# Optimization experiments

Measured on AMD Instinct MI355X. Metric: run time of the kernel, lower is better.

The kernel has to match this reference:

```python
import jax, jax.numpy as jnp
import numpy as np

B, C = 8192, 4096
P, Q, EPS = 0.8, 2.0, 0.01


def setup_inputs() -> dict:
    key = jax.random.key(0)
    k1, k2 = jax.random.split(key)
    outputs = jax.random.normal(k1, (B, C), dtype=jnp.float32)
    targets = jax.random.randint(k2, (B,), 0, C)
    return {"outputs": outputs, "targets": targets}


def reference(outputs, targets):
    num_classes = outputs.shape[1]
    # accumulated class counts for this batch (torch loop over unique targets == bincount)
    acc = jax.ops.segment_sum(
        jnp.ones_like(targets, dtype=outputs.dtype), targets, num_segments=num_classes
    )
    acc = jnp.clip(acc, 1.0)  # clamp(min=1)
    onehot = jax.nn.one_hot(targets, num_classes, dtype=outputs.dtype)  # [B, C]

    # mitigation factor: gather rows of the implicit CxC ratio matrix by target
    # ratio[b, j] = acc[j] / acc[targets[b]]
    ratio = acc[None, :] / acc[targets][:, None]  # [B, C]
    mitigation = jnp.where(ratio < 1.0, ratio ** P, 1.0)

    # compensation factor on detached softmax scores
    scores = jax.nn.softmax(jax.lax.stop_gradient(outputs), axis=1)  # [B, C]
    self_scores = jnp.take_along_axis(scores, targets[:, None], axis=1)  # [B, 1]
    sratio = scores / jnp.clip(self_scores, EPS)
    compensation = jnp.where(sratio > 1.0, sratio ** Q, 1.0)

    seesaw = mitigation * compensation  # [B, C]
    logits = outputs + jnp.log(seesaw) * (1.0 - onehot)

    logp = jax.nn.log_softmax(logits, axis=1)
    nll = -jnp.take_along_axis(logp, targets[:, None], axis=1)[:, 0]
    return jnp.mean(nll)
```

## Files before the change

kernel.cpp:

```cpp
#include <hip/hip_runtime.h>
#include <math.h>


#define CC 4096

__device__ __forceinline__ float wave_max(float v) {
    #pragma unroll
    for (int o = 32; o > 0; o >>= 1) v = fmaxf(v, __shfl_xor(v, o, 64));
    return v;
}
__device__ __forceinline__ float wave_sum(float v) {
    #pragma unroll
    for (int o = 32; o > 0; o >>= 1) v += __shfl_xor(v, o, 64);
    return v;
}

__device__ __forceinline__ float exp4(float4& v, float m) {
    v.x = __expf(v.x - m); v.y = __expf(v.y - m);
    v.z = __expf(v.z - m); v.w = __expf(v.w - m);
    return (v.x + v.y) + (v.z + v.w);
}

__device__ __forceinline__ float zsum4(float4 e, float4 pa, float rt, float c) {
    float gx = e.x * c, gy = e.y * c, gz = e.z * c, gw = e.w * c;
    float hx = fmaxf(gx * gx * gx, gx), hy = fmaxf(gy * gy * gy, gy);
    float hz = fmaxf(gz * gz * gz, gz), hw = fmaxf(gw * gw * gw, gw);
    float mx = fminf(pa.x * rt, 1.f),  my = fminf(pa.y * rt, 1.f);
    float mz = fminf(pa.z * rt, 1.f),  mw = fminf(pa.w * rt, 1.f);
    return (hx * mx + hy * my) + (hz * mz + hw * mw);
}

__global__ __launch_bounds__(1024) void k_hist(const int* __restrict__ tg, int B,
                                               float* __restrict__ powacc) {
    __shared__ int hacc[CC];
    const int tid = threadIdx.x;
    #pragma unroll
    for (int k = 0; k < CC / 1024; ++k) hacc[tid + k * 1024] = 0;
    __syncthreads();
    const int4* __restrict__ tg4 = (const int4*)tg;
    for (int i = tid; i < B / 4; i += 1024) {
        int4 tv = tg4[i];
        atomicAdd(&hacc[tv.x], 1); atomicAdd(&hacc[tv.y], 1);
        atomicAdd(&hacc[tv.z], 1); atomicAdd(&hacc[tv.w], 1);
    }
    __syncthreads();
    #pragma unroll
    for (int k = 0; k < CC / 1024; ++k) {
        int i = tid + k * 1024;
        int a = hacc[i];
        if (a < 1) a = 1;
        powacc[i] = __powf((float)a, 0.8f);
    }
}

__global__ __launch_bounds__(256, 8) void k_row(const float* __restrict__ outp,
                                                const int* __restrict__ tg,
                                                const float* __restrict__ powacc,
                                                float* __restrict__ nll) {
    __shared__ float2 red_ms[4];
    __shared__ float  red_z[4];

    const int b   = blockIdx.x;
    const int tid = threadIdx.x;
    const int w   = tid >> 6;
    const bool lane0 = (tid & 63) == 0;

    const float LOG_EPS = -4.605170185988091f;

    const int   t    = tg[b];
    const float o_t  = outp[(size_t)b * CC + t];
    const float pa_t = powacc[t];

    const float4* __restrict__ src = (const float4*)(outp + (size_t)b * CC);
    const float4* __restrict__ pac = (const float4*)powacc;

    float4 v0 = src[tid];
    float4 v1 = src[tid + 256];
    float4 v2 = src[tid + 512];
    float4 v3 = src[tid + 768];
    float4 pa0 = pac[tid];
    float4 pa1 = pac[tid + 256];
    float4 pa2 = pac[tid + 512];
    float4 pa3 = pac[tid + 768];

    float m0 = fmaxf(fmaxf(v0.x, v0.y), fmaxf(v0.z, v0.w));
    float m1 = fmaxf(fmaxf(v1.x, v1.y), fmaxf(v1.z, v1.w));
    float m2 = fmaxf(fmaxf(v2.x, v2.y), fmaxf(v2.z, v2.w));
    float m3 = fmaxf(fmaxf(v3.x, v3.y), fmaxf(v3.z, v3.w));
    const float mlane = fmaxf(fmaxf(m0, m1), fmaxf(m2, m3));

    const float mw = wave_max(mlane);

    float s = (exp4(v0, mlane) + exp4(v1, mlane)) +
              (exp4(v2, mlane) + exp4(v3, mlane));

    float S_w = wave_sum(s * __expf(mlane - mw));
    if (lane0) red_ms[w] = make_float2(mw, S_w);
    __syncthreads();

    const float M = fmaxf(fmaxf(red_ms[0].x, red_ms[1].x),
                          fmaxf(red_ms[2].x, red_ms[3].x));
    const float S = red_ms[0].y * __expf(red_ms[0].x - M)
                  + red_ms[1].y * __expf(red_ms[1].x - M)
                  + red_ms[2].y * __expf(red_ms[2].x - M)
                  + red_ms[3].y * __expf(red_ms[3].x - M);
    const float L       = M + __logf(S);
    const float logclip = fmaxf(o_t - L, LOG_EPS);
    const float Koff    = L + logclip;

    const float c  = __expf(mlane - Koff);
    const float rt = __fdividef(1.0f, pa_t);

    float z0 = zsum4(v0, pa0, rt, c);
    float z1 = zsum4(v1, pa1, rt, c);
    float z2 = zsum4(v2, pa2, rt, c);
    float z3 = zsum4(v3, pa3, rt, c);
    float z  = wave_sum((z0 + z1) + (z2 + z3));
    if (lane0) red_z[w] = z;
    __syncthreads();

    if (tid == 0) {
        float Z = (red_z[0] + red_z[1]) + (red_z[2] + red_z[3]);
        nll[b] = Koff + __logf(Z) - o_t;
    }
}

__global__ __launch_bounds__(1024) void k_reduce(const float* __restrict__ nll,
                                                 float* __restrict__ out, int B) {
    __shared__ float red[16];
    const int tid = threadIdx.x;
    const float4* __restrict__ n4 = (const float4*)nll;
    float s = 0.f;
    for (int i = tid; i < B / 4; i += 1024) {
        float4 v = n4[i];
        s += (v.x + v.y) + (v.z + v.w);
    }
    s = wave_sum(s);
    if ((tid & 63) == 0) red[tid >> 6] = s;
    __syncthreads();
    if (tid == 0) {
        float tsum = 0.f;
        #pragma unroll
        for (int k = 0; k < 16; ++k) tsum += red[k];
        out[0] = tsum / (float)B;
    }
}

extern "C" void kernel_launch(void* const* d_in, const int* in_sizes, int n_in,
                              void* d_out, int out_size, void* d_ws, size_t ws_size,
                              hipStream_t stream) {
    const float* outp = (const float*)d_in[0];
    const int*   tg   = (const int*)d_in[1];
    float*       out  = (float*)d_out;

    const int B = in_sizes[1];

    char*  ws     = (char*)d_ws;
    float* powacc = (float*)ws;
    float* nll    = (float*)(ws + 16384);

    k_hist  <<<1, 1024, 0, stream>>>(tg, B, powacc);
    k_row   <<<B, 256, 0, stream>>>(outp, tg, powacc, nll);
    k_reduce<<<1, 1024, 0, stream>>>(nll, out, B);
}
```

Measured before the change: 34.43 us.

## Process two rows per block in seesaw loss row kernel

Each 256-thread block now handles two batch rows at once. Both rows are loaded up front, their reductions are interleaved, and each powacc vector load is shared between the two rows. This halves the block count and increases memory-level parallelism and ILP per thread, at the cost of more registers. Occupancy is traded down (launch bounds 8 to 7), and two interleaved shuffle chains replace one.

```diff
diff --git a/kernel.cpp b/kernel.cpp
--- a/kernel.cpp
+++ b/kernel.cpp
@@ -4,11 +4,6 @@
 
 #define CC 4096
 
-__device__ __forceinline__ float wave_max(float v) {
-    #pragma unroll
-    for (int o = 32; o > 0; o >>= 1) v = fmaxf(v, __shfl_xor(v, o, 64));
-    return v;
-}
 __device__ __forceinline__ float wave_sum(float v) {
     #pragma unroll
     for (int o = 32; o > 0; o >>= 1) v += __shfl_xor(v, o, 64);
@@ -53,75 +48,118 @@
     }
 }
 
-__global__ __launch_bounds__(256, 8) void k_row(const float* __restrict__ outp,
+__global__ __launch_bounds__(256, 7) void k_row(const float* __restrict__ outp,
                                                 const int* __restrict__ tg,
                                                 const float* __restrict__ powacc,
                                                 float* __restrict__ nll) {
-    __shared__ float2 red_ms[4];
-    __shared__ float  red_z[4];
-
-    const int b   = blockIdx.x;
+    __shared__ float2 redA[4], redB[4];
+    __shared__ float  rzA[4],  rzB[4];
+
+    const int rA  = blockIdx.x * 2;
+    const int rB  = rA + 1;
     const int tid = threadIdx.x;
     const int w   = tid >> 6;
     const bool lane0 = (tid & 63) == 0;
 
     const float LOG_EPS = -4.605170185988091f;
 
-    const int   t    = tg[b];
-    const float o_t  = outp[(size_t)b * CC + t];
-    const float pa_t = powacc[t];
-
-    const float4* __restrict__ src = (const float4*)(outp + (size_t)b * CC);
-    const float4* __restrict__ pac = (const float4*)powacc;
-
-    float4 v0 = src[tid];
-    float4 v1 = src[tid + 256];
-    float4 v2 = src[tid + 512];
-    float4 v3 = src[tid + 768];
-    float4 pa0 = pac[tid];
-    float4 pa1 = pac[tid + 256];
-    float4 pa2 = pac[tid + 512];
-    float4 pa3 = pac[tid + 768];
-
-    float m0 = fmaxf(fmaxf(v0.x, v0.y), fmaxf(v0.z, v0.w));
-    float m1 = fmaxf(fmaxf(v1.x, v1.y), fmaxf(v1.z, v1.w));
-    float m2 = fmaxf(fmaxf(v2.x, v2.y), fmaxf(v2.z, v2.w));
-    float m3 = fmaxf(fmaxf(v3.x, v3.y), fmaxf(v3.z, v3.w));
-    const float mlane = fmaxf(fmaxf(m0, m1), fmaxf(m2, m3));
-
-    const float mw = wave_max(mlane);
-
-    float s = (exp4(v0, mlane) + exp4(v1, mlane)) +
-              (exp4(v2, mlane) + exp4(v3, mlane));
-
-    float S_w = wave_sum(s * __expf(mlane - mw));
-    if (lane0) red_ms[w] = make_float2(mw, S_w);
-    __syncthreads();
-
-    const float M = fmaxf(fmaxf(red_ms[0].x, red_ms[1].x),
-                          fmaxf(red_ms[2].x, red_ms[3].x));
-    const float S = red_ms[0].y * __expf(red_ms[0].x - M)
-                  + red_ms[1].y * __expf(red_ms[1].x - M)
-                  + red_ms[2].y * __expf(red_ms[2].x - M)
-                  + red_ms[3].y * __expf(red_ms[3].x - M);
-    const float L       = M + __logf(S);
-    const float logclip = fmaxf(o_t - L, LOG_EPS);
-    const float Koff    = L + logclip;
-
-    const float c  = __expf(mlane - Koff);
-    const float rt = __fdividef(1.0f, pa_t);
-
-    float z0 = zsum4(v0, pa0, rt, c);
-    float z1 = zsum4(v1, pa1, rt, c);
-    float z2 = zsum4(v2, pa2, rt, c);
-    float z3 = zsum4(v3, pa3, rt, c);
-    float z  = wave_sum((z0 + z1) + (z2 + z3));
-    if (lane0) red_z[w] = z;
+    const int   tA = tg[rA],                  tB = tg[rB];
+    const float o_tA = outp[(size_t)rA * CC + tA];
+    const float o_tB = outp[(size_t)rB * CC + tB];
+    const float pa_tA = powacc[tA],           pa_tB = powacc[tB];
+
+    const float4* __restrict__ srcA = (const float4*)(outp + (size_t)rA * CC);
+    const float4* __restrict__ srcB = (const float4*)(outp + (size_t)rB * CC);
+    const float4* __restrict__ pac  = (const float4*)powacc;
+
+    float4 a0 = srcA[tid];
+    float4 a1 = srcA[tid + 256];
+    float4 a2 = srcA[tid + 512];
+    float4 a3 = srcA[tid + 768];
+    float4 b0 = srcB[tid];
+    float4 b1 = srcB[tid + 256];
+    float4 b2 = srcB[tid + 512];
+    float4 b3 = srcB[tid + 768];
+
+    float mA = fmaxf(fmaxf(fmaxf(a0.x, a0.y), fmaxf(a0.z, a0.w)),
+                     fmaxf(fmaxf(a1.x, a1.y), fmaxf(a1.z, a1.w)));
+    mA = fmaxf(mA, fmaxf(fmaxf(a2.x, a2.y), fmaxf(a2.z, a2.w)));
+    mA = fmaxf(mA, fmaxf(fmaxf(a3.x, a3.y), fmaxf(a3.z, a3.w)));
+    float mB = fmaxf(fmaxf(fmaxf(b0.x, b0.y), fmaxf(b0.z, b0.w)),
+                     fmaxf(fmaxf(b1.x, b1.y), fmaxf(b1.z, b1.w)));
+    mB = fmaxf(mB, fmaxf(fmaxf(b2.x, b2.y), fmaxf(b2.z, b2.w)));
+    mB = fmaxf(mB, fmaxf(fmaxf(b3.x, b3.y), fmaxf(b3.z, b3.w)));
+
+    float mwA = mA, mwB = mB;
+    #pragma unroll
+    for (int o = 32; o > 0; o >>= 1) {
+        mwA = fmaxf(mwA, __shfl_xor(mwA, o, 64));
+        mwB = fmaxf(mwB, __shfl_xor(mwB, o, 64));
+    }
+
+    float sA = (exp4(a0, mA) + exp4(a1, mA)) + (exp4(a2, mA) + exp4(a3, mA));
+    float sB = (exp4(b0, mB) + exp4(b1, mB)) + (exp4(b2, mB) + exp4(b3, mB));
+
+    float SA = sA * __expf(mA - mwA);
+    float SB = sB * __expf(mB - mwB);
+    #pragma unroll
+    for (int o = 32; o > 0; o >>= 1) {
+        SA += __shfl_xor(SA, o, 64);
+        SB += __shfl_xor(SB, o, 64);
+    }
+    if (lane0) { redA[w] = make_float2(mwA, SA); redB[w] = make_float2(mwB, SB); }
+    __syncthreads();
+
+    const float MA = fmaxf(fmaxf(redA[0].x, redA[1].x), fmaxf(redA[2].x, redA[3].x));
+    const float MB = fmaxf(fmaxf(redB[0].x, redB[1].x), fmaxf(redB[2].x, redB[3].x));
+    const float SSA = redA[0].y * __expf(redA[0].x - MA)
+                    + redA[1].y * __expf(redA[1].x - MA)
+                    + redA[2].y * __expf(redA[2].x - MA)
+                    + redA[3].y * __expf(redA[3].x - MA);
+    const float SSB = redB[0].y * __expf(redB[0].x - MB)
+                    + redB[1].y * __expf(redB[1].x - MB)
+                    + redB[2].y * __expf(redB[2].x - MB)
+                    + redB[3].y * __expf(redB[3].x - MB);
+    const float LA = MA + __logf(SSA);
+    const float LB = MB + __logf(SSB);
+    const float KoffA = LA + fmaxf(o_tA - LA, LOG_EPS);
+    const float KoffB = LB + fmaxf(o_tB - LB, LOG_EPS);
+    const float cA = __expf(mA - KoffA), cB = __expf(mB - KoffB);
+    const float rtA = __fdividef(1.0f, pa_tA);
+    const float rtB = __fdividef(1.0f, pa_tB);
+
+    float zA, zB;
+    {
+        float4 p = pac[tid];
+        zA = zsum4(a0, p, rtA, cA);  zB = zsum4(b0, p, rtB, cB);
+    }
+    {
+        float4 p = pac[tid + 256];
+        zA += zsum4(a1, p, rtA, cA); zB += zsum4(b1, p, rtB, cB);
+    }
+    {
+        float4 p = pac[tid + 512];
+        zA += zsum4(a2, p, rtA, cA); zB += zsum4(b2, p, rtB, cB);
+    }
+    {
+        float4 p = pac[tid + 768];
+        zA += zsum4(a3, p, rtA, cA); zB += zsum4(b3, p, rtB, cB);
+    }
+    #pragma unroll
+    for (int o = 32; o > 0; o >>= 1) {
+        zA += __shfl_xor(zA, o, 64);
+        zB += __shfl_xor(zB, o, 64);
+    }
+    if (lane0) { rzA[w] = zA; rzB[w] = zB; }
     __syncthreads();
 
     if (tid == 0) {
-        float Z = (red_z[0] + red_z[1]) + (red_z[2] + red_z[3]);
-        nll[b] = Koff + __logf(Z) - o_t;
+        float Z = (rzA[0] + rzA[1]) + (rzA[2] + rzA[3]);
+        nll[rA] = KoffA + __logf(Z) - o_tA;
+    }
+    if (tid == 64) {
+        float Z = (rzB[0] + rzB[1]) + (rzB[2] + rzB[3]);
+        nll[rB] = KoffB + __logf(Z) - o_tB;
     }
 }
 
@@ -160,6 +198,6 @@
     float* nll    = (float*)(ws + 16384);
 
     k_hist  <<<1, 1024, 0, stream>>>(tg, B, powacc);
-    k_row   <<<B, 256, 0, stream>>>(outp, tg, powacc, nll);
+    k_row   <<<B / 2, 256, 0, stream>>>(outp, tg, powacc, nll);
     k_reduce<<<1, 1024, 0, stream>>>(nll, out, B);
 }
```

Result: slower. 36.27 us (+5.4%).

## Process eight rows per block with double-buffered register prefetch of next row

Applied to the files above, without the earlier changes.

Each block of k_row now handles eight consecutive rows instead of one. It alternates two register sets so the next row's float4 loads are issued before the current row's reductions and barriers. The grid shrinks to B/8 blocks and the occupancy hint drops from 8 to 4 blocks per CU, which keeps register pressure manageable with the extra buffers. The powacc float4 values are reloaded from cache for every row instead of held in registers. The aim is to hide global load latency behind the sync-heavy per-row reductions and cut block launch overhead, at the cost of fewer resident waves and more serial work per block.

```diff
diff --git a/kernel.cpp b/kernel.cpp
--- a/kernel.cpp
+++ b/kernel.cpp
@@ -3,6 +3,7 @@
 
 
 #define CC 4096
+#define NR 8
 
 __device__ __forceinline__ float wave_max(float v) {
     #pragma unroll
@@ -53,76 +54,70 @@
     }
 }
 
-__global__ __launch_bounds__(256, 8) void k_row(const float* __restrict__ outp,
+#define PRE_LOAD(U0, U1, U2, U3, RIDX) { \
+    const float4* __restrict__ srcn = (const float4*)(outp + (size_t)(b0 + (RIDX)) * CC); \
+    U0 = srcn[tid]; U1 = srcn[tid + 256]; U2 = srcn[tid + 512]; U3 = srcn[tid + 768]; }
+
+#define ROW_BODY(A0, A1, A2, A3, RIDX, PRE) { \
+    const int   t_   = tg[b0 + (RIDX)];                        \
+    const float ot_  = outp[(size_t)(b0 + (RIDX)) * CC + t_]; \
+    const float pat_ = powacc[t_]; \
+    PRE \
+    float q0 = fmaxf(fmaxf(A0.x, A0.y), fmaxf(A0.z, A0.w)); \
+    float q1 = fmaxf(fmaxf(A1.x, A1.y), fmaxf(A1.z, A1.w)); \
+    float q2 = fmaxf(fmaxf(A2.x, A2.y), fmaxf(A2.z, A2.w)); \
+    float q3 = fmaxf(fmaxf(A3.x, A3.y), fmaxf(A3.z, A3.w)); \
+    const float mlane = fmaxf(fmaxf(q0, q1), fmaxf(q2, q3)); \
+    const float mw = wave_max(mlane); \
+    float s_ = (exp4(A0, mlane) + exp4(A1, mlane)) + (exp4(A2, mlane) + exp4(A3, mlane)); \
+    float Sw = wave_sum(s_ * __expf(mlane - mw)); \
+    if (lane0) red_ms[w] = make_float2(mw, Sw); \
+    __syncthreads(); \
+    const float M_ = fmaxf(fmaxf(red_ms[0].x, red_ms[1].x), fmaxf(red_ms[2].x, red_ms[3].x)); \
+    const float S_ = red_ms[0].y * __expf(red_ms[0].x - M_) \
+                   + red_ms[1].y * __expf(red_ms[1].x - M_) \
+                   + red_ms[2].y * __expf(red_ms[2].x - M_) \
+                   + red_ms[3].y * __expf(red_ms[3].x - M_); \
+    const float L_   = M_ + __logf(S_); \
+    const float Koff = L_ + fmaxf(ot_ - L_, LOG_EPS); \
+    const float cf   = __expf(mlane - Koff); \
+    const float rt_  = __fdividef(1.0f, pat_); \
+    float z0 = zsum4(A0, pac[tid      ], rt_, cf); \
+    float z1 = zsum4(A1, pac[tid + 256], rt_, cf); \
+    float z2 = zsum4(A2, pac[tid + 512], rt_, cf); \
+    float z3 = zsum4(A3, pac[tid + 768], rt_, cf); \
+    float z_ = wave_sum((z0 + z1) + (z2 + z3)); \
+    if (lane0) red_z[w] = z_; \
+    __syncthreads(); \
+    if (tid == 0) nll[b0 + (RIDX)] = Koff + __logf((red_z[0] + red_z[1]) + (red_z[2] + red_z[3])) - ot_; \
+}
+
+__global__ __launch_bounds__(256, 4) void k_row(const float* __restrict__ outp,
                                                 const int* __restrict__ tg,
                                                 const float* __restrict__ powacc,
                                                 float* __restrict__ nll) {
     __shared__ float2 red_ms[4];
     __shared__ float  red_z[4];
 
-    const int b   = blockIdx.x;
+    const int b0  = blockIdx.x * NR;
     const int tid = threadIdx.x;
     const int w   = tid >> 6;
     const bool lane0 = (tid & 63) == 0;
 
     const float LOG_EPS = -4.605170185988091f;
-
-    const int   t    = tg[b];
-    const float o_t  = outp[(size_t)b * CC + t];
-    const float pa_t = powacc[t];
-
-    const float4* __restrict__ src = (const float4*)(outp + (size_t)b * CC);
     const float4* __restrict__ pac = (const float4*)powacc;
 
-    float4 v0 = src[tid];
-    float4 v1 = src[tid + 256];
-    float4 v2 = src[tid + 512];
-    float4 v3 = src[tid + 768];
-    float4 pa0 = pac[tid];
-    float4 pa1 = pac[tid + 256];
-    float4 pa2 = pac[tid + 512];
-    float4 pa3 = pac[tid + 768];
+    float4 a0, a1, a2, a3, u0, u1, u2, u3;
+    PRE_LOAD(a0, a1, a2, a3, 0)
 
-    float m0 = fmaxf(fmaxf(v0.x, v0.y), fmaxf(v0.z, v0.w));
-    float m1 = fmaxf(fmaxf(v1.x, v1.y), fmaxf(v1.z, v1.w));
-    float m2 = fmaxf(fmaxf(v2.x, v2.y), fmaxf(v2.z, v2.w));
-    float m3 = fmaxf(fmaxf(v3.x, v3.y), fmaxf(v3.z, v3.w));
-    const float mlane = fmaxf(fmaxf(m0, m1), fmaxf(m2, m3));
-
-    const float mw = wave_max(mlane);
-
-    float s = (exp4(v0, mlane) + exp4(v1, mlane)) +
-              (exp4(v2, mlane) + exp4(v3, mlane));
-
-    float S_w = wave_sum(s * __expf(mlane - mw));
-    if (lane0) red_ms[w] = make_float2(mw, S_w);
-    __syncthreads();
-
-    const float M = fmaxf(fmaxf(red_ms[0].x, red_ms[1].x),
-                          fmaxf(red_ms[2].x, red_ms[3].x));
-    const float S = red_ms[0].y * __expf(red_ms[0].x - M)
-                  + red_ms[1].y * __expf(red_ms[1].x - M)
-                  + red_ms[2].y * __expf(red_ms[2].x - M)
-                  + red_ms[3].y * __expf(red_ms[3].x - M);
-    const float L       = M + __logf(S);
-    const float logclip = fmaxf(o_t - L, LOG_EPS);
-    const float Koff    = L + logclip;
-
-    const float c  = __expf(mlane - Koff);
-    const float rt = __fdividef(1.0f, pa_t);
-
-    float z0 = zsum4(v0, pa0, rt, c);
-    float z1 = zsum4(v1, pa1, rt, c);
-    float z2 = zsum4(v2, pa2, rt, c);
-    float z3 = zsum4(v3, pa3, rt, c);
-    float z  = wave_sum((z0 + z1) + (z2 + z3));
-    if (lane0) red_z[w] = z;
-    __syncthreads();
-
-    if (tid == 0) {
-        float Z = (red_z[0] + red_z[1]) + (red_z[2] + red_z[3]);
-        nll[b] = Koff + __logf(Z) - o_t;
-    }
+    ROW_BODY(a0, a1, a2, a3, 0, PRE_LOAD(u0, u1, u2, u3, 1))
+    ROW_BODY(u0, u1, u2, u3, 1, PRE_LOAD(a0, a1, a2, a3, 2))
+    ROW_BODY(a0, a1, a2, a3, 2, PRE_LOAD(u0, u1, u2, u3, 3))
+    ROW_BODY(u0, u1, u2, u3, 3, PRE_LOAD(a0, a1, a2, a3, 4))
+    ROW_BODY(a0, a1, a2, a3, 4, PRE_LOAD(u0, u1, u2, u3, 5))
+    ROW_BODY(u0, u1, u2, u3, 5, PRE_LOAD(a0, a1, a2, a3, 6))
+    ROW_BODY(a0, a1, a2, a3, 6, PRE_LOAD(u0, u1, u2, u3, 7))
+    ROW_BODY(u0, u1, u2, u3, 7, )
 }
 
 __global__ __launch_bounds__(1024) void k_reduce(const float* __restrict__ nll,
@@ -160,6 +155,6 @@
     float* nll    = (float*)(ws + 16384);
 
     k_hist  <<<1, 1024, 0, stream>>>(tg, B, powacc);
-    k_row   <<<B, 256, 0, stream>>>(outp, tg, powacc, nll);
+    k_row   <<<B / NR, 256, 0, stream>>>(outp, tg, powacc, nll);
     k_reduce<<<1, 1024, 0, stream>>>(nll, out, B);
 }
```

After: 40.89 us. 1.19x slower.
